# Optimization experiments

Hardware: AMD Instinct MI355X
Metric: run time of the kernel (lower is better)

The kernel has to match this reference:

```python
import jax, jax.numpy as jnp
import numpy as np

N = 50000   # nodes
E = 800000  # edges
IND = 128   # in_dim
HID = 128   # num_hidden
NH = 4      # heads
HD = HID // NH
L = 2       # num_layers
SLOPE = 0.2


def setup_inputs() -> dict:
    key = jax.random.key(0)
    ks = jax.random.split(key, 32)
    rn = lambda k, shp, s=1.0: jax.random.normal(k, shp, jnp.float32) * s
    W = 0.08  # weight scale (xavier-ish)
    return {
        "x_t": rn(ks[0], (N, IND)),
        "time_embed": rn(ks[1], (N, HID)),
        "src": jax.random.randint(ks[2], (E,), 0, N),
        "dst": jax.random.randint(ks[3], (E,), 0, N),
        "W_init": rn(ks[4], (IND + HID, HID), W), "b_init": jnp.zeros((HID,), jnp.float32),
        "Wsrc_down": rn(ks[5], (L, HID, HID), W), "bsrc_down": jnp.zeros((L, HID), jnp.float32),
        "Wdst_down": rn(ks[6], (L, HID, HID), W), "bdst_down": jnp.zeros((L, HID), jnp.float32),
        "attn_down": rn(ks[7], (L, NH, HD), W), "bout_down": jnp.zeros((L, HID), jnp.float32),
        "Wsrc_mid": rn(ks[8], (HID, HID), W), "bsrc_mid": jnp.zeros((HID,), jnp.float32),
        "Wdst_mid": rn(ks[9], (HID, HID), W), "bdst_mid": jnp.zeros((HID,), jnp.float32),
        "attn_mid": rn(ks[10], (NH, HD), W), "bout_mid": jnp.zeros((HID,), jnp.float32),
        "Wsrc_up": rn(ks[11], (L, 2 * HID, HID), W), "bsrc_up": jnp.zeros((L, HID), jnp.float32),
        "Wdst_up": rn(ks[12], (L, 2 * HID, HID), W), "bdst_up": jnp.zeros((L, HID), jnp.float32),
        "attn_up": rn(ks[13], (L, NH, HD), W), "bout_up": jnp.zeros((L, HID), jnp.float32),
        "W_fin": rn(ks[14], (HID, HID), W), "b_fin": jnp.zeros((HID,), jnp.float32),
    }


def gatv2_layer(h, Wsrc, bsrc, Wdst, bdst, attn, bout, src, dst):
    # GATv2Conv (DGL semantics, eval mode / no dropout), flatten(1) included.
    fs = (h @ Wsrc + bsrc).reshape(-1, NH, HD)  # [N,H,D]
    fd = (h @ Wdst + bdst).reshape(-1, NH, HD)
    e = jax.nn.leaky_relu(fs[src] + fd[dst], SLOPE)           # [E,H,D]
    logits = jnp.einsum('ehd,hd->eh', e, attn)                # [E,H]
    m = jax.ops.segment_max(logits, dst, num_segments=N)      # [N,H]
    m = jnp.where(jnp.isfinite(m), m, 0.0)                    # zero-in-degree safety
    p = jnp.exp(logits - m[dst])                              # [E,H]
    s = jax.ops.segment_sum(p, dst, num_segments=N)           # [N,H]
    alpha = p / (s[dst] + 1e-9)                               # edge softmax per dst
    out = jax.ops.segment_sum(alpha[:, :, None] * fs[src], dst, num_segments=N)
    out = out.reshape(-1, HID) + bout
    return jax.nn.gelu(out)


def reference(x_t, time_embed, src, dst,
              W_init, b_init,
              Wsrc_down, bsrc_down, Wdst_down, bdst_down, attn_down, bout_down,
              Wsrc_mid, bsrc_mid, Wdst_mid, bdst_mid, attn_mid, bout_mid,
              Wsrc_up, bsrc_up, Wdst_up, bdst_up, attn_up, bout_up,
              W_fin, b_fin):
    h = jnp.concatenate([x_t, time_embed], axis=1)
    h = jax.nn.gelu(h @ W_init + b_init)
    skips = []
    for i in range(L):
        skips.append(h)
        h = gatv2_layer(h, Wsrc_down[i], bsrc_down[i], Wdst_down[i], bdst_down[i],
                        attn_down[i], bout_down[i], src, dst)
    h = gatv2_layer(h, Wsrc_mid, bsrc_mid, Wdst_mid, bdst_mid, attn_mid, bout_mid, src, dst)
    for i in range(L):
        h = jnp.concatenate([h, skips[L - 1 - i]], axis=1)
        h = gatv2_layer(h, Wsrc_up[i], bsrc_up[i], Wdst_up[i], bdst_up[i],
                        attn_up[i], bout_up[i], src, dst)
    out = h @ W_fin + b_fin
    return (out, h)
```

## Files before the change

kernel.cpp:

```cpp
#include <hip/hip_runtime.h>
#include <hip/hip_bf16.h>
#include <math.h>

#define HIDDIM 128
#define MT 64

typedef float f32x4 __attribute__((ext_vector_type(4)));
typedef short bf16x8 __attribute__((ext_vector_type(8)));

__device__ inline float gelu_f(float x) {
  float x3 = x * x * x;
  return 0.5f * x * (1.0f + tanhf(0.7978845608028654f * (x + 0.044715f * x3)));
}

__device__ inline void split_bf16(float a, unsigned short& hi, unsigned short& lo) {
  unsigned u = __float_as_uint(a);
  unsigned r = (u + 0x7FFFu + ((u >> 16) & 1u)) & 0xFFFF0000u;
  hi = (unsigned short)(r >> 16);
  float rem = a - __uint_as_float(r);
  unsigned u2 = __float_as_uint(rem);
  lo = (unsigned short)((u2 + 0x7FFFu + ((u2 >> 16) & 1u)) >> 16);
}

__global__ void detect_dtype(const unsigned short* __restrict__ raw, int* __restrict__ flag) {
  __shared__ int cnt;
  if (threadIdx.x == 0) cnt = 0;
  __syncthreads();
  int c = 0;
  for (int i = threadIdx.x; i < 8192; i += 256) {
    int ex = (raw[i] >> 7) & 0xFF;
    if (ex >= 0xC0) c++;
  }
  atomicAdd(&cnt, c);
  __syncthreads();
  if (threadIdx.x == 0) flag[0] = (cnt > 64) ? 1 : 0;
}

__global__ void cvt_to_f32_2(const void* __restrict__ in0, const void* __restrict__ in1,
                             float* __restrict__ out0, float* __restrict__ out1,
                             int n, const int* __restrict__ flag) {
  int i = blockIdx.x * 256 + threadIdx.x;
  if (i < n) {
    out0[i] = flag[0] ? ((const float*)in0)[i]
                      : __bfloat162float(((const __hip_bfloat16*)in0)[i]);
  } else if (i < 2 * n) {
    int j = i - n;
    out1[j] = flag[0] ? ((const float*)in1)[j]
                      : __bfloat162float(((const __hip_bfloat16*)in1)[j]);
  }
}

#define NITEMS 14
struct StageArgs {
  const void* src[NITEMS];
  int off[NITEMS];
  int n[NITEMS];
  int blk0[NITEMS];
};
__global__ void stage_params(StageArgs a, float* __restrict__ params,
                             const int* __restrict__ flag) {
  int b = blockIdx.x;
  int it = 0;
  while (it + 1 < NITEMS && a.blk0[it + 1] <= b) ++it;
  int i = (b - a.blk0[it]) * 256 + threadIdx.x;
  if (i < a.n[it]) {
    params[a.off[it] + i] = flag[0]
        ? ((const float*)a.src[it])[i]
        : __bfloat162float(((const __hip_bfloat16*)a.src[it])[i]);
  }
}

#define NSPLIT 12
struct SplitArgs {
  const void* src[NSPLIT];
  int eoff[NSPLIT];
  int soff[NSPLIT];
  int K[NSPLIT];
  int blk0[NSPLIT];
};
__global__ void split_weights(SplitArgs a,
                              unsigned short* __restrict__ whi,
                              unsigned short* __restrict__ wlo,
                              const int* __restrict__ flag) {
  int b = blockIdx.x, it = 0;
  while (it + 1 < NSPLIT && a.blk0[it + 1] <= b) ++it;
  int i = (b - a.blk0[it]) * 256 + threadIdx.x;
  int K = a.K[it];
  if (i < K * 128) {
    float v = flag[0]
        ? ((const float*)a.src[it])[a.eoff[it] + i]
        : __bfloat162float(((const __hip_bfloat16*)a.src[it])[a.eoff[it] + i]);
    int k = i >> 7, col = i & 127;
    unsigned short h, lo;
    split_bf16(v, h, lo);
    int o = a.soff[it] + col * K + k;
    whi[o] = h;
    wlo[o] = lo;
  }
}

template <int KT, int FUSED, int ACT>
__global__ __launch_bounds__(256) void gemm_mfma(
    const float* __restrict__ A1, const float* __restrict__ A2,
    const unsigned short* __restrict__ Whi0, const unsigned short* __restrict__ Wlo0,
    const unsigned short* __restrict__ Whi1, const unsigned short* __restrict__ Wlo1,
    const float* __restrict__ b0, const float* __restrict__ b1,
    float* __restrict__ C0, float* __restrict__ C1, int M) {
  constexpr int K = KT * 32;
  constexpr int CT = FUSED ? 8 : 4;
  __shared__ __align__(16) unsigned short AsH[64][40];
  __shared__ __align__(16) unsigned short AsL[64][40];
  const int t = threadIdx.x;
  const int w = t >> 6, l = t & 63;
  const int m0 = blockIdx.x * 64;
  const int rbase = (w & 1) * 32;
  const int chalf = w >> 1;
  const unsigned short* whi = (FUSED && chalf) ? Whi1 : Whi0;
  const unsigned short* wlo = (FUSED && chalf) ? Wlo1 : Wlo0;
  const int cbase = FUSED ? 0 : chalf * 64;
  float* Cw = (FUSED && chalf) ? C1 : C0;
  const float* bw = (FUSED && chalf) ? b1 : b0;
  const int lr = l & 15;
  const int lk = l >> 4;

  float4 Areg[2];
#pragma unroll
  for (int i = 0; i < 2; ++i) {
    int f = t + i * 256, row = f >> 3, kc = f & 7;
    int gr = min(m0 + row, M - 1);
    Areg[i] = *(const float4*)&A1[(size_t)gr * 128 + kc * 4];
  }

  f32x4 acc[2][CT];
#pragma unroll
  for (int rt = 0; rt < 2; ++rt)
#pragma unroll
    for (int ct = 0; ct < CT; ++ct) acc[rt][ct] = (f32x4){0.f, 0.f, 0.f, 0.f};

  for (int s = 0; s < KT; ++s) {
    __syncthreads();
#pragma unroll
    for (int i = 0; i < 2; ++i) {
      int f = t + i * 256, row = f >> 3, kc = f & 7;
      float4 v = Areg[i];
      ushort4 hh, ll;
      split_bf16(v.x, hh.x, ll.x);
      split_bf16(v.y, hh.y, ll.y);
      split_bf16(v.z, hh.z, ll.z);
      split_bf16(v.w, hh.w, ll.w);
      *(ushort4*)&AsH[row][kc * 4] = hh;
      *(ushort4*)&AsL[row][kc * 4] = ll;
    }
    if (s + 1 < KT) {
      int sn = s + 1;
      const float* Ab = (KT == 8 && sn >= 4) ? A2 : A1;
      int krel = (sn & 3) * 32;
#pragma unroll
      for (int i = 0; i < 2; ++i) {
        int f = t + i * 256, row = f >> 3, kc = f & 7;
        int gr = min(m0 + row, M - 1);
        Areg[i] = *(const float4*)&Ab[(size_t)gr * 128 + krel + kc * 4];
      }
    }
    bf16x8 bh[CT], bl[CT];
#pragma unroll
    for (int ct = 0; ct < CT; ++ct) {
      size_t off = (size_t)(cbase + ct * 16 + lr) * K + s * 32 + lk * 8;
      bh[ct] = *(const bf16x8*)&whi[off];
      bl[ct] = *(const bf16x8*)&wlo[off];
    }
    __syncthreads();
    bf16x8 ah[2], al[2];
#pragma unroll
    for (int rt = 0; rt < 2; ++rt) {
      int row = rbase + rt * 16 + lr;
      ah[rt] = *(const bf16x8*)&AsH[row][lk * 8];
      al[rt] = *(const bf16x8*)&AsL[row][lk * 8];
    }
#pragma unroll
    for (int rt = 0; rt < 2; ++rt)
#pragma unroll
      for (int ct = 0; ct < CT; ++ct) {
        acc[rt][ct] = __builtin_amdgcn_mfma_f32_16x16x32_bf16(ah[rt], bh[ct], acc[rt][ct], 0, 0, 0);
        acc[rt][ct] = __builtin_amdgcn_mfma_f32_16x16x32_bf16(ah[rt], bl[ct], acc[rt][ct], 0, 0, 0);
        acc[rt][ct] = __builtin_amdgcn_mfma_f32_16x16x32_bf16(al[rt], bh[ct], acc[rt][ct], 0, 0, 0);
      }
  }

#pragma unroll
  for (int ct = 0; ct < CT; ++ct) {
    int col = cbase + ct * 16 + lr;
    float bias = bw[col];
#pragma unroll
    for (int rt = 0; rt < 2; ++rt) {
      int rowb = m0 + rbase + rt * 16 + lk * 4;
#pragma unroll
      for (int r = 0; r < 4; ++r) {
        int row = rowb + r;
        if (row < M) {
          float v = acc[rt][ct][r] + bias;
          if (ACT) v = gelu_f(v);
          Cw[(size_t)row * 128 + col] = v;
        }
      }
    }
  }
}

__global__ void count_deg(const int* __restrict__ dst, int* __restrict__ deg, int E) {
  int e = blockIdx.x * 256 + threadIdx.x;
  if (e < E) atomicAdd(&deg[dst[e]], 1);
}

__global__ __launch_bounds__(1024) void scan_blocks(
    const int* __restrict__ deg, int* __restrict__ rowptr,
    int* __restrict__ cursor, int* __restrict__ bsum, int N) {
  __shared__ int buf[1024];
  int i = blockIdx.x * 1024 + threadIdx.x;
  int v = (i < N) ? deg[i] : 0;
  buf[threadIdx.x] = v;
  __syncthreads();
  for (int off = 1; off < 1024; off <<= 1) {
    int add = (threadIdx.x >= (unsigned)off) ? buf[threadIdx.x - off] : 0;
    __syncthreads();
    buf[threadIdx.x] += add;
    __syncthreads();
  }
  int excl = buf[threadIdx.x] - v;
  if (i < N) { rowptr[i] = excl; cursor[i] = excl; }
  if (threadIdx.x == 1023) bsum[blockIdx.x] = buf[1023];
}

__global__ __launch_bounds__(1024) void scan_partials(int* __restrict__ bsum, int nb) {
  __shared__ int buf[1024];
  int v = (threadIdx.x < (unsigned)nb) ? bsum[threadIdx.x] : 0;
  buf[threadIdx.x] = v;
  __syncthreads();
  for (int off = 1; off < 1024; off <<= 1) {
    int add = (threadIdx.x >= (unsigned)off) ? buf[threadIdx.x - off] : 0;
    __syncthreads();
    buf[threadIdx.x] += add;
    __syncthreads();
  }
  int excl = buf[threadIdx.x] - v;
  if (threadIdx.x < (unsigned)nb) bsum[threadIdx.x] = excl;
  if (threadIdx.x == 1023) bsum[nb] = buf[1023];
}

__global__ void add_offsets(int* __restrict__ rowptr, int* __restrict__ cursor,
                            const int* __restrict__ bsum, int N, int nb) {
  int i = blockIdx.x * 256 + threadIdx.x;
  if (i < N) {
    int add = bsum[i >> 10];
    rowptr[i] += add;
    cursor[i] += add;
  }
  if (i == 0) rowptr[N] = bsum[nb];
}

__global__ void place_edges(const int* __restrict__ src, const int* __restrict__ dst,
                            int* __restrict__ cursor, int* __restrict__ colsrc, int E) {
  int e = blockIdx.x * 256 + threadIdx.x;
  if (e < E) {
    int pos = atomicAdd(&cursor[dst[e]], 1);
    colsrc[pos] = src[e];
  }
}

__global__ __launch_bounds__(256) void gat_agg(
    const float* __restrict__ fs, const float* __restrict__ fd,
    const int* __restrict__ rowptr, const int* __restrict__ colsrc,
    const float* __restrict__ attn, const float* __restrict__ bout,
    float* __restrict__ hout, int N, int E) {
  int wv = threadIdx.x >> 6, lane = threadIdx.x & 63;
  int n = blockIdx.x * 4 + wv;
  if (n >= N) return;
  int half = lane >> 5;
  int fb = (lane & 31) * 4;
  float4 fdv = *(const float4*)&fd[(size_t)n * HIDDIM + fb];
  float a0 = attn[fb], a1 = attn[fb + 1], a2 = attn[fb + 2], a3 = attn[fb + 3];
  int e0 = rowptr[n], e1 = rowptr[n + 1];
  e0 = max(0, min(e0, E));
  e1 = max(e0, min(e1, E));
  float s = 0.f, ax = 0.f, ay = 0.f, az = 0.f, aw = 0.f;
  for (int c0 = e0; c0 < e1; c0 += 64) {
    int cn = min(64, e1 - c0);
    int myidx = (lane < cn) ? colsrc[c0 + lane] : 0;
    myidx = ((unsigned)myidx < (unsigned)N) ? myidx : 0;
    int iters = (cn + 3) >> 2;
    for (int it = 0; it < iters; ++it) {
      int jA = 4 * it + half;
      int jB = jA + 2;
      int sA = __shfl(myidx, min(jA, cn - 1));
      int sB = __shfl(myidx, min(jB, cn - 1));
      float4 fA = *(const float4*)&fs[(size_t)sA * HIDDIM + fb];
      float4 fB = *(const float4*)&fs[(size_t)sB * HIDDIM + fb];
      float v0, v1, v2, v3, lA, lB;
      v0 = fA.x + fdv.x; v0 = v0 > 0.f ? v0 : 0.2f * v0;
      v1 = fA.y + fdv.y; v1 = v1 > 0.f ? v1 : 0.2f * v1;
      v2 = fA.z + fdv.z; v2 = v2 > 0.f ? v2 : 0.2f * v2;
      v3 = fA.w + fdv.w; v3 = v3 > 0.f ? v3 : 0.2f * v3;
      lA = fmaf(v0, a0, fmaf(v1, a1, fmaf(v2, a2, v3 * a3)));
      v0 = fB.x + fdv.x; v0 = v0 > 0.f ? v0 : 0.2f * v0;
      v1 = fB.y + fdv.y; v1 = v1 > 0.f ? v1 : 0.2f * v1;
      v2 = fB.z + fdv.z; v2 = v2 > 0.f ? v2 : 0.2f * v2;
      v3 = fB.w + fdv.w; v3 = v3 > 0.f ? v3 : 0.2f * v3;
      lB = fmaf(v0, a0, fmaf(v1, a1, fmaf(v2, a2, v3 * a3)));
      lA += __shfl_xor(lA, 1); lA += __shfl_xor(lA, 2); lA += __shfl_xor(lA, 4);
      lB += __shfl_xor(lB, 1); lB += __shfl_xor(lB, 2); lB += __shfl_xor(lB, 4);
      lA = fminf(lA, 60.f);
      lB = fminf(lB, 60.f);
      float pA = (jA < cn) ? __expf(lA) : 0.f;
      float pB = (jB < cn) ? __expf(lB) : 0.f;
      s += pA + pB;
      ax = fmaf(pA, fA.x, fmaf(pB, fB.x, ax));
      ay = fmaf(pA, fA.y, fmaf(pB, fB.y, ay));
      az = fmaf(pA, fA.z, fmaf(pB, fB.z, az));
      aw = fmaf(pA, fA.w, fmaf(pB, fB.w, aw));
    }
  }
  s += __shfl_xor(s, 32);
  ax += __shfl_xor(ax, 32); ay += __shfl_xor(ay, 32);
  az += __shfl_xor(az, 32); aw += __shfl_xor(aw, 32);
  if (half == 0) {
    float inv = 1.f / (s + 1e-9f);
    float o0 = gelu_f(fmaf(ax, inv, bout[fb]));
    float o1 = gelu_f(fmaf(ay, inv, bout[fb + 1]));
    float o2 = gelu_f(fmaf(az, inv, bout[fb + 2]));
    float o3 = gelu_f(fmaf(aw, inv, bout[fb + 3]));
    *(float4*)&hout[(size_t)n * HIDDIM + fb] = make_float4(o0, o1, o2, o3);
  }
}

__global__ void store_out(const float* __restrict__ og, const float* __restrict__ h,
                          void* __restrict__ dout, int n, const int* __restrict__ flag) {
  int i = blockIdx.x * 256 + threadIdx.x;
  if (i >= n) return;
  if (flag[0]) {
    ((float*)dout)[i] = og[i];
    ((float*)dout)[n + i] = h[i];
  } else {
    ((__hip_bfloat16*)dout)[i] = __float2bfloat16(og[i]);
    ((__hip_bfloat16*)dout)[n + i] = __float2bfloat16(h[i]);
  }
}

#define PB_INIT    0
#define PBSRC_DOWN 128
#define PBDST_DOWN 384
#define PATTN_DOWN 640
#define PBOUT_DOWN 896
#define PBSRC_MID  1152
#define PBDST_MID  1280
#define PATTN_MID  1408
#define PBOUT_MID  1536
#define PBSRC_UP   1664
#define PBDST_UP   1920
#define PATTN_UP   2176
#define PBOUT_UP   2432
#define PB_FIN     2688
#define PARAMS_TOTAL 2816

#define SP_W_INIT    0
#define SP_WSRC_D0   32768
#define SP_WSRC_D1   49152
#define SP_WDST_D0   65536
#define SP_WDST_D1   81920
#define SP_WSRC_MID  98304
#define SP_WDST_MID  114688
#define SP_WSRC_U0   131072
#define SP_WSRC_U1   163840
#define SP_WDST_U0   196608
#define SP_WDST_U1   229376
#define SP_W_FIN     262144
#define SPLIT_TOTAL  278528

extern "C" void kernel_launch(void* const* d_in, const int* in_sizes, int n_in,
                              void* d_out, int out_size, void* d_ws, size_t ws_size,
                              hipStream_t stream) {
  const int N = in_sizes[1] / HIDDIM;
  const int E = in_sizes[2];
  const int* src = (const int*)d_in[2];
  const int* dst = (const int*)d_in[3];

  char* p = (char*)d_ws;
  auto carve = [&](size_t bytes) {
    void* r = (void*)p;
    p += (bytes + 255) & ~(size_t)255;
    return r;
  };
  int* flag     = (int*)carve(256);
  float* params = (float*)carve((size_t)PARAMS_TOTAL * 4);
  unsigned short* whi = (unsigned short*)carve((size_t)SPLIT_TOTAL * 2);
  unsigned short* wlo = (unsigned short*)carve((size_t)SPLIT_TOTAL * 2);
  int* deg      = (int*)carve((size_t)N * 4);
  int* rowptr   = (int*)carve((size_t)(N + 1) * 4);
  int* cursor   = (int*)carve((size_t)N * 4);
  int* bsum     = (int*)carve(1032 * 4);
  int* colsrc   = (int*)carve((size_t)E * 4);
  float* hA     = (float*)carve((size_t)N * HIDDIM * 4);
  float* hB     = (float*)carve((size_t)N * HIDDIM * 4);
  float* hC     = (float*)carve((size_t)N * HIDDIM * 4);
  float* fs     = (float*)carve((size_t)N * HIDDIM * 4);
  float* fd     = (float*)carve((size_t)N * HIDDIM * 4);

  detect_dtype<<<1, 256, 0, stream>>>((const unsigned short*)d_in[0], flag);

  static const int idx[NITEMS] = {5, 7, 9, 10, 11, 13, 15, 16, 17, 19, 21, 22, 23, 25};
  static const int off[NITEMS] = {
    PB_INIT, PBSRC_DOWN, PBDST_DOWN, PATTN_DOWN, PBOUT_DOWN,
    PBSRC_MID, PBDST_MID, PATTN_MID, PBOUT_MID,
    PBSRC_UP, PBDST_UP, PATTN_UP, PBOUT_UP, PB_FIN};
  static const int cnt[NITEMS] = {
    128, 256, 256, 256, 256, 128, 128, 128, 128, 256, 256, 256, 256, 128};
  StageArgs sa;
  int nb = 0;
  for (int i = 0; i < NITEMS; ++i) {
    sa.src[i] = d_in[idx[i]];
    sa.off[i] = off[i];
    sa.n[i] = cnt[i];
    sa.blk0[i] = nb;
    nb += (cnt[i] + 255) / 256;
  }
  stage_params<<<nb, 256, 0, stream>>>(sa, params, flag);

  static const int widx[NSPLIT]  = {4, 6, 6, 8, 8, 12, 14, 18, 18, 20, 20, 24};
  static const int weoff[NSPLIT] = {0, 0, 16384, 0, 16384, 0, 0, 0, 32768, 0, 32768, 0};
  static const int wsoff[NSPLIT] = {
    SP_W_INIT, SP_WSRC_D0, SP_WSRC_D1, SP_WDST_D0, SP_WDST_D1,
    SP_WSRC_MID, SP_WDST_MID, SP_WSRC_U0, SP_WSRC_U1, SP_WDST_U0, SP_WDST_U1,
    SP_W_FIN};
  static const int wK[NSPLIT] = {256, 128, 128, 128, 128, 128, 128, 256, 256, 256, 256, 128};
  SplitArgs spa;
  int snb = 0;
  for (int i = 0; i < NSPLIT; ++i) {
    spa.src[i] = d_in[widx[i]];
    spa.eoff[i] = weoff[i];
    spa.soff[i] = wsoff[i];
    spa.K[i] = wK[i];
    spa.blk0[i] = snb;
    snb += (wK[i] * 128 + 255) / 256;
  }
  split_weights<<<snb, 256, 0, stream>>>(spa, whi, wlo, flag);

  float* xc = fs;
  float* tc = fd;
  cvt_to_f32_2<<<(2 * N * HIDDIM + 255) / 256, 256, 0, stream>>>(
      d_in[0], d_in[1], xc, tc, N * HIDDIM, flag);

  hipMemsetAsync(deg, 0, (size_t)N * 4, stream);
  count_deg<<<(E + 255) / 256, 256, 0, stream>>>(dst, deg, E);
  int nsb = (N + 1023) / 1024;
  scan_blocks<<<nsb, 1024, 0, stream>>>(deg, rowptr, cursor, bsum, N);
  scan_partials<<<1, 1024, 0, stream>>>(bsum, nsb);
  add_offsets<<<(N + 255) / 256, 256, 0, stream>>>(rowptr, cursor, bsum, N, nsb);
  place_edges<<<(E + 255) / 256, 256, 0, stream>>>(src, dst, cursor, colsrc, E);

  dim3 gb((N + MT - 1) / MT);
  dim3 ga((N + 3) / 4);
  const float* P = params;

  gemm_mfma<8, 0, 1><<<gb, 256, 0, stream>>>(
      xc, tc, whi + SP_W_INIT, wlo + SP_W_INIT, nullptr, nullptr,
      P + PB_INIT, nullptr, hA, nullptr, N);

  auto gat_layer = [&](const float* ha, const float* hb, int spsrc, int spdst,
                       const float* bsrc, const float* bdst,
                       const float* attn, const float* bout, float* hout) {
    if (hb)
      gemm_mfma<8, 1, 0><<<gb, 256, 0, stream>>>(
          ha, hb, whi + spsrc, wlo + spsrc, whi + spdst, wlo + spdst,
          bsrc, bdst, fs, fd, N);
    else
      gemm_mfma<4, 1, 0><<<gb, 256, 0, stream>>>(
          ha, nullptr, whi + spsrc, wlo + spsrc, whi + spdst, wlo + spdst,
          bsrc, bdst, fs, fd, N);
    gat_agg<<<ga, 256, 0, stream>>>(fs, fd, rowptr, colsrc, attn, bout, hout, N, E);
  };

  gat_layer(hA, nullptr, SP_WSRC_D0, SP_WDST_D0, P + PBSRC_DOWN, P + PBDST_DOWN,
            P + PATTN_DOWN, P + PBOUT_DOWN, hB);
  gat_layer(hB, nullptr, SP_WSRC_D1, SP_WDST_D1, P + PBSRC_DOWN + 128,
            P + PBDST_DOWN + 128, P + PATTN_DOWN + 128, P + PBOUT_DOWN + 128, hC);
  gat_layer(hC, nullptr, SP_WSRC_MID, SP_WDST_MID, P + PBSRC_MID, P + PBDST_MID,
            P + PATTN_MID, P + PBOUT_MID, hC);
  gat_layer(hC, hB, SP_WSRC_U0, SP_WDST_U0, P + PBSRC_UP, P + PBDST_UP,
            P + PATTN_UP, P + PBOUT_UP, hC);
  gat_layer(hC, hA, SP_WSRC_U1, SP_WDST_U1, P + PBSRC_UP + 128, P + PBDST_UP + 128,
            P + PATTN_UP + 128, P + PBOUT_UP + 128, hC);

  float* outg = hB;
  gemm_mfma<4, 0, 0><<<gb, 256, 0, stream>>>(
      hC, nullptr, whi + SP_W_FIN, wlo + SP_W_FIN, nullptr, nullptr,
      P + PB_FIN, nullptr, outg, nullptr, N);
  store_out<<<(N * HIDDIM + 255) / 256, 256, 0, stream>>>(outg, hC, d_out, N * HIDDIM, flag);
}
```

Baseline: 965.2 us.

## Load A fragments directly from global into registers, dropping LDS staging in GEMM

The MFMA GEMM no longer stages split bf16 hi/lo A tiles through shared memory with two barriers per K step. Each lane now loads its own 8 floats per row-tile straight from global memory, splits them pairwise into packed hi/lo words, and feeds the MFMAs. The K loop is fully unrolled and launch bounds request 3 blocks per CU. This removes the LDS traffic and syncs, but the same A data is reloaded redundantly by the wave pairs that share rows, and the explicit prefetch that overlapped loads with compute is gone.

Result: slower. 1.023 ms (+6.0%).

```diff
diff --git a/kernel.cpp b/kernel.cpp
--- a/kernel.cpp
+++ b/kernel.cpp
@@ -6,6 +6,7 @@
 #define MT 64
 
 typedef float f32x4 __attribute__((ext_vector_type(4)));
+typedef int i32x4 __attribute__((ext_vector_type(4)));
 typedef short bf16x8 __attribute__((ext_vector_type(8)));
 
 __device__ inline float gelu_f(float x) {
@@ -20,6 +21,19 @@
   float rem = a - __uint_as_float(r);
   unsigned u2 = __float_as_uint(rem);
   lo = (unsigned short)((u2 + 0x7FFFu + ((u2 >> 16) & 1u)) >> 16);
+}
+
+__device__ inline void split_pair(float a0, float a1, unsigned& hp, unsigned& lp) {
+  unsigned u0 = __float_as_uint(a0), u1 = __float_as_uint(a1);
+  unsigned r0 = (u0 + 0x7FFFu + ((u0 >> 16) & 1u)) & 0xFFFF0000u;
+  unsigned r1 = (u1 + 0x7FFFu + ((u1 >> 16) & 1u)) & 0xFFFF0000u;
+  hp = (r0 >> 16) | r1;
+  float m0 = a0 - __uint_as_float(r0);
+  float m1 = a1 - __uint_as_float(r1);
+  unsigned v0 = __float_as_uint(m0), v1 = __float_as_uint(m1);
+  unsigned s0 = v0 + 0x7FFFu + ((v0 >> 16) & 1u);
+  unsigned s1 = (v1 + 0x7FFFu + ((v1 >> 16) & 1u)) & 0xFFFF0000u;
+  lp = (s0 >> 16) | s1;
 }
 
 __global__ void detect_dtype(const unsigned short* __restrict__ raw, int* __restrict__ flag) {
@@ -100,7 +114,7 @@
 }
 
 template <int KT, int FUSED, int ACT>
-__global__ __launch_bounds__(256) void gemm_mfma(
+__global__ __launch_bounds__(256, 3) void gemm_mfma(
     const float* __restrict__ A1, const float* __restrict__ A2,
     const unsigned short* __restrict__ Whi0, const unsigned short* __restrict__ Wlo0,
     const unsigned short* __restrict__ Whi1, const unsigned short* __restrict__ Wlo1,
@@ -108,8 +122,6 @@
     float* __restrict__ C0, float* __restrict__ C1, int M) {
   constexpr int K = KT * 32;
   constexpr int CT = FUSED ? 8 : 4;
-  __shared__ __align__(16) unsigned short AsH[64][40];
-  __shared__ __align__(16) unsigned short AsL[64][40];
   const int t = threadIdx.x;
   const int w = t >> 6, l = t & 63;
   const int m0 = blockIdx.x * 64;
@@ -123,13 +135,9 @@
   const int lr = l & 15;
   const int lk = l >> 4;
 
-  float4 Areg[2];
-#pragma unroll
-  for (int i = 0; i < 2; ++i) {
-    int f = t + i * 256, row = f >> 3, kc = f & 7;
-    int gr = min(m0 + row, M - 1);
-    Areg[i] = *(const float4*)&A1[(size_t)gr * 128 + kc * 4];
-  }
+  int arow[2];
+#pragma unroll
+  for (int rt = 0; rt < 2; ++rt) arow[rt] = min(m0 + rbase + rt * 16 + lr, M - 1);
 
   f32x4 acc[2][CT];
 #pragma unroll
@@ -137,31 +145,27 @@
 #pragma unroll
     for (int ct = 0; ct < CT; ++ct) acc[rt][ct] = (f32x4){0.f, 0.f, 0.f, 0.f};
 
+#pragma unroll
   for (int s = 0; s < KT; ++s) {
-    __syncthreads();
-#pragma unroll
-    for (int i = 0; i < 2; ++i) {
-      int f = t + i * 256, row = f >> 3, kc = f & 7;
-      float4 v = Areg[i];
-      ushort4 hh, ll;
-      split_bf16(v.x, hh.x, ll.x);
-      split_bf16(v.y, hh.y, ll.y);
-      split_bf16(v.z, hh.z, ll.z);
-      split_bf16(v.w, hh.w, ll.w);
-      *(ushort4*)&AsH[row][kc * 4] = hh;
-      *(ushort4*)&AsL[row][kc * 4] = ll;
+    const float* Ab = (KT == 8 && s >= 4) ? A2 : A1;
+    const int krel = (KT == 8 ? (s & 3) : s) * 32 + lk * 8;
+
+    bf16x8 ah[2], al[2];
+#pragma unroll
+    for (int rt = 0; rt < 2; ++rt) {
+      const float* ap = &Ab[(size_t)arow[rt] * 128 + krel];
+      float4 v0 = *(const float4*)ap;
+      float4 v1 = *(const float4*)(ap + 4);
+      i32x4 hv, lv;
+      unsigned hp, lp;
+      split_pair(v0.x, v0.y, hp, lp); hv[0] = (int)hp; lv[0] = (int)lp;
+      split_pair(v0.z, v0.w, hp, lp); hv[1] = (int)hp; lv[1] = (int)lp;
+      split_pair(v1.x, v1.y, hp, lp); hv[2] = (int)hp; lv[2] = (int)lp;
+      split_pair(v1.z, v1.w, hp, lp); hv[3] = (int)hp; lv[3] = (int)lp;
+      ah[rt] = __builtin_bit_cast(bf16x8, hv);
+      al[rt] = __builtin_bit_cast(bf16x8, lv);
     }
-    if (s + 1 < KT) {
-      int sn = s + 1;
-      const float* Ab = (KT == 8 && sn >= 4) ? A2 : A1;
-      int krel = (sn & 3) * 32;
-#pragma unroll
-      for (int i = 0; i < 2; ++i) {
-        int f = t + i * 256, row = f >> 3, kc = f & 7;
-        int gr = min(m0 + row, M - 1);
-        Areg[i] = *(const float4*)&Ab[(size_t)gr * 128 + krel + kc * 4];
-      }
-    }
+
     bf16x8 bh[CT], bl[CT];
 #pragma unroll
     for (int ct = 0; ct < CT; ++ct) {
@@ -169,14 +173,7 @@
       bh[ct] = *(const bf16x8*)&whi[off];
       bl[ct] = *(const bf16x8*)&wlo[off];
     }
-    __syncthreads();
-    bf16x8 ah[2], al[2];
-#pragma unroll
-    for (int rt = 0; rt < 2; ++rt) {
-      int row = rbase + rt * 16 + lr;
-      ah[rt] = *(const bf16x8*)&AsH[row][lk * 8];
-      al[rt] = *(const bf16x8*)&AsL[row][lk * 8];
-    }
+
 #pragma unroll
     for (int rt = 0; rt < 2; ++rt)
 #pragma unroll
```
